# Optimization experiments

Measured on AMD Instinct MI355X. Metric: run time of the kernel, lower is better.

The kernel has to match this reference:

```python
import jax, jax.numpy as jnp
import numpy as np

N = 50000   # number of nodes
E = 25000   # number of hyperedges
IN = 256
OUT = 256
L = 32      # incidence list width (padded with 0)
NEG = -9e15  # matches torch's -9000000000000000.0 (fits in fp32)


def setup_inputs() -> dict:
    key = jax.random.key(0)
    k1, k2, k3, k4, k5 = jax.random.split(key, 5)
    x = jax.random.normal(k1, (N, IN), dtype=jnp.float32)
    seq = jax.random.randint(k2, (E, L), 0, N)      # node ids per hyperedge
    useq = jax.random.randint(k3, (N, L), 0, E)     # edge ids per node
    stdv = 1.0 / np.sqrt(IN)
    W1 = jax.random.uniform(k4, (IN, OUT), minval=-stdv, maxval=stdv, dtype=jnp.float32)
    W2 = jax.random.uniform(k5, (OUT, OUT), minval=-stdv, maxval=stdv, dtype=jnp.float32)
    return {"x": x, "seq": seq, "useq": useq, "W1": W1, "W2": W2}


def _mask_softmax_weights(idx):
    # softmax over where(idx>0, 1, -9e15): uniform weights over non-padding slots
    logits = jnp.where(idx > 0, 1.0, NEG).astype(jnp.float32)
    return jax.nn.softmax(logits, axis=1)


def reference(x, seq, useq, W1, W2):
    x1 = x @ W1                                   # [N, OUT]
    w = _mask_softmax_weights(seq)                # [E, L]
    edge = jnp.einsum('elc,el->ec', x1[seq], w)   # gather + weighted reduce -> [E, OUT]
    # F.dropout is identity in eval mode
    edge = jax.nn.relu(edge)
    e1 = edge @ W2                                # [E, OUT]
    uw = _mask_softmax_weights(useq)              # [N, L]
    node = jnp.einsum('nlc,nl->nc', e1[useq], uw) # [N, OUT]
    return node
```

## Files before the change

### kernel.cpp

```cpp
#include <hip/hip_runtime.h>

constexpr int N_NODES = 50000;
constexpr int N_EDGES = 25000;
constexpr int C = 256;
constexpr int L = 32;

__device__ ushort W1T_g[C * C];
__device__ ushort W2T_g[C * C];

__device__ __forceinline__ ushort f2bf(float f) {
    union { float f; unsigned int u; } c; c.f = f;
    unsigned int r = c.u + 0x7FFFu + ((c.u >> 16) & 1u);
    return (ushort)(r >> 16);
}
__device__ __forceinline__ float bflo(unsigned int u) {
    union { unsigned int x; float f; } c; c.x = u << 16; return c.f;
}
__device__ __forceinline__ float bfhi(unsigned int u) {
    union { unsigned int x; float f; } c; c.x = u & 0xFFFF0000u; return c.f;
}
__device__ __forceinline__ void acc_uint4(float* acc, const uint4 v) {
    acc[0] += bflo(v.x); acc[1] += bfhi(v.x);
    acc[2] += bflo(v.y); acc[3] += bfhi(v.y);
    acc[4] += bflo(v.z); acc[5] += bfhi(v.z);
    acc[6] += bflo(v.w); acc[7] += bfhi(v.w);
}

__global__ __launch_bounds__(256) void convert_x_kernel(
    const float* __restrict__ x, ushort* __restrict__ xb)
{
    const size_t i = ((size_t)blockIdx.x * 256 + threadIdx.x) * 4;
    const float4 v = *reinterpret_cast<const float4*>(x + i);
    ushort4 o;
    o.x = f2bf(v.x); o.y = f2bf(v.y); o.z = f2bf(v.z); o.w = f2bf(v.w);
    *reinterpret_cast<ushort4*>(xb + i) = o;
}

__global__ __launch_bounds__(256) void wconv_kernel(
    const float* __restrict__ W1, const float* __restrict__ W2)
{
    const float* W  = blockIdx.z ? W2 : W1;
    ushort* WT      = blockIdx.z ? W2T_g : W1T_g;
    __shared__ float t[64][65];
    const int rr = threadIdx.x >> 6;
    const int cc = threadIdx.x & 63;
    const int br = blockIdx.x * 64;
    const int bc = blockIdx.y * 64;
#pragma unroll
    for (int i = 0; i < 16; ++i) {
        const int row = i * 4 + rr;
        t[row][cc] = W[(size_t)(br + row) * C + bc + cc];
    }
    __syncthreads();
#pragma unroll
    for (int i = 0; i < 16; ++i) {
        const int n = i * 4 + rr;
        WT[(size_t)(bc + n) * C + br + cc] = f2bf(t[cc][n]);
    }
}

__global__ __launch_bounds__(256) void gather_edge_kernel(
    const ushort* __restrict__ src, const int* __restrict__ idx,
    ushort* __restrict__ dst, int nrows)
{
    const int row = blockIdx.x * 8 + (threadIdx.x >> 5);
    const int ln  = threadIdx.x & 31;
    if (row >= nrows) return;

    const int myid = idx[(size_t)row * L + ln];
    const unsigned long long b = __ballot(myid > 0);
    const unsigned int halfmask = (unsigned int)(b >> (threadIdx.x & 32));
    const int cnt = __popc(halfmask);

    float acc[8] = {0.f, 0.f, 0.f, 0.f, 0.f, 0.f, 0.f, 0.f};
#pragma unroll
    for (int l = 0; l < L; ++l) {
        const int id = __shfl(myid, l, 32);
        const uint4 v = *reinterpret_cast<const uint4*>(
            src + (size_t)id * C + ln * 8);
        acc_uint4(acc, v);
    }
    const uint4 v0 = *reinterpret_cast<const uint4*>(src + ln * 8);
    float x0[8];
    x0[0] = bflo(v0.x); x0[1] = bfhi(v0.x); x0[2] = bflo(v0.y); x0[3] = bfhi(v0.y);
    x0[4] = bflo(v0.z); x0[5] = bfhi(v0.z); x0[6] = bflo(v0.w); x0[7] = bfhi(v0.w);

    const float corr = (cnt == 0) ? 0.f : (float)(L - cnt);
    const float inv  = (cnt == 0) ? (1.f / (float)L) : (1.f / (float)cnt);

    ushort* d = dst + (size_t)row * C + ln * 8;
    uint4 o;
    o.x = (unsigned)f2bf((acc[0] - corr * x0[0]) * inv) |
          ((unsigned)f2bf((acc[1] - corr * x0[1]) * inv) << 16);
    o.y = (unsigned)f2bf((acc[2] - corr * x0[2]) * inv) |
          ((unsigned)f2bf((acc[3] - corr * x0[3]) * inv) << 16);
    o.z = (unsigned)f2bf((acc[4] - corr * x0[4]) * inv) |
          ((unsigned)f2bf((acc[5] - corr * x0[5]) * inv) << 16);
    o.w = (unsigned)f2bf((acc[6] - corr * x0[6]) * inv) |
          ((unsigned)f2bf((acc[7] - corr * x0[7]) * inv) << 16);
    *reinterpret_cast<uint4*>(d) = o;
}

__global__ __launch_bounds__(256) void gather_node_kernel(
    const ushort* __restrict__ src, const int* __restrict__ idx,
    float* __restrict__ dst, int nrows)
{
    constexpr int CH = 64, NCHUNK = 4;
    constexpr int LPR = CH / 8;
    constexpr int RPB = 256 / LPR;
    const int chunk = blockIdx.x & (NCHUNK - 1);
    const int rb    = (int)(blockIdx.x / NCHUNK) * RPB;
    const int t     = threadIdx.x;

    __shared__ int sidx[RPB][33];
#pragma unroll
    for (int i = 0; i < (RPB * L) / 256; ++i) {
        const int flat = i * 256 + t;
        const int r = flat >> 5, l = flat & 31;
        sidx[r][l] = (rb + r < nrows) ? idx[(size_t)(rb + r) * L + l] : 0;
    }
    __syncthreads();

    const int r   = t / LPR;
    const int ch  = chunk * CH + (t % LPR) * 8;
    const int row = rb + r;
    if (row >= nrows) return;

    float acc[8] = {0.f, 0.f, 0.f, 0.f, 0.f, 0.f, 0.f, 0.f};
    int cnt = 0;
#pragma unroll
    for (int l = 0; l < L; ++l) {
        const int id = sidx[r][l];
        cnt += (id > 0) ? 1 : 0;
        const uint4 v = *reinterpret_cast<const uint4*>(
            src + (size_t)id * C + ch);
        acc_uint4(acc, v);
    }
    const uint4 v0 = *reinterpret_cast<const uint4*>(src + ch);
    float x0[8];
    x0[0] = bflo(v0.x); x0[1] = bfhi(v0.x); x0[2] = bflo(v0.y); x0[3] = bfhi(v0.y);
    x0[4] = bflo(v0.z); x0[5] = bfhi(v0.z); x0[6] = bflo(v0.w); x0[7] = bfhi(v0.w);

    const float corr = (cnt == 0) ? 0.f : (float)(L - cnt);
    const float inv  = (cnt == 0) ? (1.f / (float)L) : (1.f / (float)cnt);

    float* d = dst + (size_t)row * C + ch;
    float4 o0 = {(acc[0] - corr * x0[0]) * inv, (acc[1] - corr * x0[1]) * inv,
                 (acc[2] - corr * x0[2]) * inv, (acc[3] - corr * x0[3]) * inv};
    float4 o1 = {(acc[4] - corr * x0[4]) * inv, (acc[5] - corr * x0[5]) * inv,
                 (acc[6] - corr * x0[6]) * inv, (acc[7] - corr * x0[7]) * inv};
    *reinterpret_cast<float4*>(d)     = o0;
    *reinterpret_cast<float4*>(d + 4) = o1;
}

typedef __attribute__((ext_vector_type(8))) short bf16x8;
typedef __attribute__((ext_vector_type(4))) float f32x4;

template <bool RELU>
__global__ __launch_bounds__(256) void gemm_mfma_kernel(
    const ushort* __restrict__ A, int which_w,
    ushort* __restrict__ Cmat, int M)
{
    const ushort* __restrict__ BT = which_w ? W2T_g : W1T_g;
    const int wave  = threadIdx.x >> 6;
    const int lane  = threadIdx.x & 63;
    const int quad  = lane >> 4;
    const int l16   = lane & 15;
    const int base  = (blockIdx.x * 4 + wave) * 32;
    const int nbase = blockIdx.y * 128;

    int m0 = base + l16;      if (m0 > M - 1) m0 = M - 1;
    int m1 = base + 16 + l16; if (m1 > M - 1) m1 = M - 1;

    f32x4 acc[2][8];
    const f32x4 zero = {0.f, 0.f, 0.f, 0.f};
#pragma unroll
    for (int p = 0; p < 2; ++p)
#pragma unroll
        for (int t = 0; t < 8; ++t) acc[p][t] = zero;

    const ushort* a0 = A + (size_t)m0 * C + quad * 8;
    const ushort* a1 = A + (size_t)m1 * C + quad * 8;
    const ushort* br = BT + (size_t)(nbase + l16) * C + quad * 8;

#pragma unroll
    for (int k0 = 0; k0 < C; k0 += 32) {
        const bf16x8 av0 = *reinterpret_cast<const bf16x8*>(a0 + k0);
        const bf16x8 av1 = *reinterpret_cast<const bf16x8*>(a1 + k0);
#pragma unroll
        for (int t = 0; t < 8; ++t) {
            const bf16x8 b = *reinterpret_cast<const bf16x8*>(
                br + (size_t)t * 16 * C + k0);
            acc[0][t] = __builtin_amdgcn_mfma_f32_16x16x32_bf16(av0, b, acc[0][t], 0, 0, 0);
            acc[1][t] = __builtin_amdgcn_mfma_f32_16x16x32_bf16(av1, b, acc[1][t], 0, 0, 0);
        }
    }

#pragma unroll
    for (int p = 0; p < 2; ++p)
#pragma unroll
    for (int t = 0; t < 8; ++t)
#pragma unroll
    for (int r = 0; r < 4; ++r) {
        const int gm = base + p * 16 + quad * 4 + r;
        if (gm < M) {
            float v = acc[p][t][r];
            if (RELU) v = fmaxf(v, 0.f);
            Cmat[(size_t)gm * C + nbase + t * 16 + l16] = f2bf(v);
        }
    }
}

extern "C" void kernel_launch(void* const* d_in, const int* in_sizes, int n_in,
                              void* d_out, int out_size, void* d_ws, size_t ws_size,
                              hipStream_t stream) {
    const float* x    = (const float*)d_in[0];
    const int*   seq  = (const int*)d_in[1];
    const int*   useq = (const int*)d_in[2];
    const float* W1   = (const float*)d_in[3];
    const float* W2   = (const float*)d_in[4];
    float* out = (float*)d_out;

    ushort* xb   = (ushort*)d_ws;
    ushort* tmp1 = xb + (size_t)N_NODES * C;
    ushort* edge = tmp1 + (size_t)N_EDGES * C;

    convert_x_kernel<<<dim3((N_NODES * C) / (256 * 4)), dim3(256), 0, stream>>>(x, xb);
    wconv_kernel<<<dim3(4, 4, 2), dim3(256), 0, stream>>>(W1, W2);

    gather_edge_kernel<<<dim3((N_EDGES + 7) / 8), dim3(256), 0, stream>>>(
        xb, seq, tmp1, N_EDGES);

    const dim3 ggrid((N_EDGES + 127) / 128, 2);
    gemm_mfma_kernel<true><<<ggrid, dim3(256), 0, stream>>>(tmp1, 0, edge, N_EDGES);
    gemm_mfma_kernel<false><<<ggrid, dim3(256), 0, stream>>>(edge, 1, tmp1, N_EDGES);

    const int rblk2 = (N_NODES + 31) / 32;
    gather_node_kernel<<<dim3(4 * rblk2), dim3(256), 0, stream>>>(
        tmp1, useq, out, N_NODES);
}
```

Baseline: 281.2 us.

## Assign node-gather column chunks per XCC via atomic work counters

The node gather kernel now reads the XCC id of the block and claims a row group for a column chunk tied to that XCC through global atomic counters, stealing from other chunks once its own is used up. Each XCC's L2 then mostly holds one 64-column slice of the edge table, which should raise cache hit rates for the random gathers. Output stores become nontemporal so the large fp32 result does not evict gather data. The cost is one atomic per block plus a barrier, and correctness depends on the counters being reset in convert_x_kernel on every call.

```diff
diff --git a/kernel.cpp b/kernel.cpp
--- a/kernel.cpp
+++ b/kernel.cpp
@@ -7,6 +7,11 @@
 
 __device__ ushort W1T_g[C * C];
 __device__ ushort W2T_g[C * C];
+
+__device__ int chunk_cnt_g[4];
+
+typedef __attribute__((ext_vector_type(8))) short bf16x8;
+typedef __attribute__((ext_vector_type(4))) float f32x4;
 
 __device__ __forceinline__ ushort f2bf(float f) {
     union { float f; unsigned int u; } c; c.f = f;
@@ -26,9 +31,16 @@
     acc[6] += bflo(v.w); acc[7] += bfhi(v.w);
 }
 
+__device__ __forceinline__ int get_xcc_id() {
+    int x;
+    asm volatile("s_getreg_b32 %0, hwreg(HW_REG_XCC_ID)" : "=s"(x));
+    return x & 7;
+}
+
 __global__ __launch_bounds__(256) void convert_x_kernel(
     const float* __restrict__ x, ushort* __restrict__ xb)
 {
+    if (blockIdx.x == 0 && threadIdx.x < 4) chunk_cnt_g[threadIdx.x] = 0;
     const size_t i = ((size_t)blockIdx.x * 256 + threadIdx.x) * 4;
     const float4 v = *reinterpret_cast<const float4*>(x + i);
     ushort4 o;
@@ -108,9 +120,24 @@
     constexpr int CH = 64, NCHUNK = 4;
     constexpr int LPR = CH / 8;
     constexpr int RPB = 256 / LPR;
-    const int chunk = blockIdx.x & (NCHUNK - 1);
-    const int rb    = (int)(blockIdx.x / NCHUNK) * RPB;
-    const int t     = threadIdx.x;
+    constexpr int RBLK = (N_NODES + RPB - 1) / RPB;
+    const int t = threadIdx.x;
+
+    __shared__ int s_chunk, s_rg;
+    if (t == 0) {
+        const int xcc = get_xcc_id();
+        int c = xcc & (NCHUNK - 1), rg = -1;
+#pragma unroll
+        for (int i = 0; i < NCHUNK; ++i) {
+            const int cc = (xcc + i) & (NCHUNK - 1);
+            const int u = atomicAdd(&chunk_cnt_g[cc], 1);
+            if (u < RBLK) { c = cc; rg = u; break; }
+        }
+        s_chunk = c; s_rg = rg;
+    }
+    __syncthreads();
+    const int chunk = s_chunk;
+    const int rb    = s_rg * RPB;
 
     __shared__ int sidx[RPB][33];
 #pragma unroll
@@ -145,16 +172,13 @@
     const float inv  = (cnt == 0) ? (1.f / (float)L) : (1.f / (float)cnt);
 
     float* d = dst + (size_t)row * C + ch;
-    float4 o0 = {(acc[0] - corr * x0[0]) * inv, (acc[1] - corr * x0[1]) * inv,
-                 (acc[2] - corr * x0[2]) * inv, (acc[3] - corr * x0[3]) * inv};
-    float4 o1 = {(acc[4] - corr * x0[4]) * inv, (acc[5] - corr * x0[5]) * inv,
-                 (acc[6] - corr * x0[6]) * inv, (acc[7] - corr * x0[7]) * inv};
-    *reinterpret_cast<float4*>(d)     = o0;
-    *reinterpret_cast<float4*>(d + 4) = o1;
-}
-
-typedef __attribute__((ext_vector_type(8))) short bf16x8;
-typedef __attribute__((ext_vector_type(4))) float f32x4;
+    f32x4 o0 = {(acc[0] - corr * x0[0]) * inv, (acc[1] - corr * x0[1]) * inv,
+                (acc[2] - corr * x0[2]) * inv, (acc[3] - corr * x0[3]) * inv};
+    f32x4 o1 = {(acc[4] - corr * x0[4]) * inv, (acc[5] - corr * x0[5]) * inv,
+                (acc[6] - corr * x0[6]) * inv, (acc[7] - corr * x0[7]) * inv};
+    __builtin_nontemporal_store(o0, reinterpret_cast<f32x4*>(d));
+    __builtin_nontemporal_store(o1, reinterpret_cast<f32x4*>(d) + 1);
+}
 
 template <bool RELU>
 __global__ __launch_bounds__(256) void gemm_mfma_kernel(
```

After: 289.8 us. +3.1%, slower.
